# Kernel optimization log

Measured on AMD Instinct MI355X. Metric: run time of the kernel, lower is better.

## Reference

```python
import jax, jax.numpy as jnp
import numpy as np

B, S, D = 2, 2048, 1024
H, DK = 16, 64            # n_heads, d_k = d_model // n_heads
EXP = 4                   # pattern-separation expand_factor
ED = DK * EXP             # expanded_dim = 256
TOPK = 32                 # top-k kept after ReLU expansion
ALPHA = 0.05
TNT = 1.0                 # trace_norm_target


def setup_inputs() -> dict:
    key = jax.random.key(0)
    ks = jax.random.split(key, 8)
    sc = 1.0 / np.sqrt(D)
    x = jax.random.normal(ks[0], (B, S, D), jnp.float32)
    W_q = jax.random.normal(ks[1], (D, D), jnp.float32) * sc
    W_k = jax.random.normal(ks[2], (D, D), jnp.float32) * sc
    W_v = jax.random.normal(ks[3], (D, D), jnp.float32) * sc
    W_o = jax.random.normal(ks[4], (D, D), jnp.float32) * sc
    # trace buffers (non-zero so the trace read path actually matters)
    traces = jax.random.normal(ks[5], (H, DK, DK), jnp.float32) * 0.02
    value_traces = jax.random.normal(ks[6], (H, ED, DK), jnp.float32) * 0.02
    # frozen random expansion projection (dentate gyrus), W / sqrt(d_k)
    W_expand = jax.random.normal(ks[7], (DK, ED), jnp.float32) / np.sqrt(DK)
    return dict(x=x, W_q=W_q, W_k=W_k, W_v=W_v, W_o=W_o,
                traces=traces, value_traces=value_traces, W_expand=W_expand)


def _eff_alpha(T):
    # alpha / (1 + ||T_h||_F / trace_norm_target), shape (1, H, 1, 1)
    norms = jnp.sqrt(jnp.sum(T * T, axis=(1, 2)))
    return (ALPHA / (1.0 + norms / TNT)).reshape(1, -1, 1, 1)


def _forward(x, W_q, W_k, W_v, W_o, traces, value_traces, W_expand):
    b, s, d = x.shape
    def proj(W):
        return jnp.einsum('bsd,de->bse', x, W).reshape(b, s, H, DK).transpose(0, 2, 1, 3)
    Q, K, V = proj(W_q), proj(W_k), proj(W_v)  # (B, H, S, DK)

    scores = jnp.einsum('bhqd,bhkd->bhqk', Q, K)
    # score trace bias: alpha_eff * (Q @ T @ K^T)
    QT = jnp.einsum('bhqd,hde->bhqe', Q, traces)
    trace_scores = jnp.einsum('bhqe,bhke->bhqk', QT, K)
    scores = (scores + _eff_alpha(traces) * trace_scores) / np.sqrt(DK)
    A = jax.nn.softmax(scores, axis=-1)
    out = jnp.einsum('bhqk,bhkd->bhqd', A, V)

    # value trace read with use_key_q shift: address with previous token's Q
    Q_addr = jnp.concatenate([jnp.zeros_like(Q[:, :, :1, :]), Q[:, :, :-1, :]], axis=2)
    # pattern separation: frozen random expansion + ReLU + top-k sparsify
    Q_exp = jax.nn.relu(jnp.einsum('bhsd,de->bhse', Q_addr, W_expand))  # (B,H,S,ED)
    kth = jax.lax.top_k(Q_exp, TOPK)[0][..., -1:]
    Q_sparse = jnp.where(Q_exp >= kth, Q_exp, 0.0)  # == scatter of top-k vals (ties at 0 contribute 0)
    stored = jnp.einsum('bhse,hed->bhsd', Q_sparse, value_traces)
    out = out + _eff_alpha(value_traces) * stored

    out = out.transpose(0, 2, 1, 3).reshape(b, s, d)
    return jnp.einsum('bsd,de->bse', out, W_o)


def reference(x, W_q, W_k, W_v, W_o, traces, value_traces, W_expand):
    return _forward(x, W_q, W_k, W_v, W_o, traces, value_traces, W_expand)
```

## Files before the change

kernel.cpp:

```cpp
#include <hip/hip_runtime.h>
#include <stdint.h>

#define Bn 2
#define Sn 2048
#define Dn 1024
#define Hn 16
#define DKn 64
#define EDn 256

typedef __attribute__((ext_vector_type(8))) short bvec8;
typedef __attribute__((ext_vector_type(4))) float fvec4;

#define MFMA(a, b, c) __builtin_amdgcn_mfma_f32_16x16x32_bf16(a, b, c, 0, 0, 0)

__device__ __forceinline__ float b2f(unsigned short u) {
  return __uint_as_float(((unsigned)u) << 16);
}
__device__ __forceinline__ unsigned short f2b(float x) {
  unsigned u = __float_as_uint(x);
  u += 0x7fffu + ((u >> 16) & 1u);
  return (unsigned short)(u >> 16);
}
__device__ __forceinline__ void g2l(const unsigned short* g, unsigned short* l) {
  __builtin_amdgcn_global_load_lds(
      (const __attribute__((address_space(1))) void*)g,
      (__attribute__((address_space(3))) void*)l, 16, 0, 0);
}

__global__ __launch_bounds__(256) void k_alphas(
    const float* __restrict__ traces, const float* __restrict__ vtr,
    float* __restrict__ alphas) {
  int blk = blockIdx.x;
  const float* base;
  int n;
  if (blk < 16) { base = traces + blk * DKn * DKn; n = DKn * DKn; }
  else          { base = vtr + (blk - 16) * EDn * DKn; n = EDn * DKn; }
  float s = 0.f;
  for (int i = threadIdx.x; i < n; i += 256) { float v = base[i]; s += v * v; }
  __shared__ float red[256];
  red[threadIdx.x] = s;
  __syncthreads();
  for (int off = 128; off > 0; off >>= 1) {
    if (threadIdx.x < off) red[threadIdx.x] += red[threadIdx.x + off];
    __syncthreads();
  }
  if (threadIdx.x == 0) alphas[blk] = 0.05f / (1.f + sqrtf(red[0]));
}

__global__ __launch_bounds__(256) void k_trW(
    const float* __restrict__ w0, const float* __restrict__ w1,
    const float* __restrict__ w2, const float* __restrict__ w3,
    unsigned short* __restrict__ dst) {
  int z = blockIdx.z;
  const float* src = (z == 0) ? w0 : ((z == 1) ? w1 : ((z == 2) ? w2 : w3));
  unsigned short* d = dst + (size_t)z * Dn * Dn;
  __shared__ unsigned short Tl[64][72];
  int tid = threadIdx.x;
  int k0 = blockIdx.y * 64, n0 = blockIdx.x * 64;
#pragma unroll
  for (int i = 0; i < 4; ++i) {
    int q = tid + 256 * i;
    int kr = q >> 4, c4 = q & 15;
    float4 v = *(const float4*)&src[(size_t)(k0 + kr) * Dn + n0 + 4 * c4];
    ushort4 u;
    u.x = f2b(v.x); u.y = f2b(v.y); u.z = f2b(v.z); u.w = f2b(v.w);
    *(ushort4*)&Tl[kr][4 * c4] = u;
  }
  __syncthreads();
#pragma unroll
  for (int i = 0; i < 4; ++i) {
    int q = tid + 256 * i;
    int nr = q >> 4, c4 = q & 15;
    ushort4 u;
    u.x = Tl[4 * c4 + 0][nr]; u.y = Tl[4 * c4 + 1][nr];
    u.z = Tl[4 * c4 + 2][nr]; u.w = Tl[4 * c4 + 3][nr];
    *(ushort4*)&d[(size_t)(n0 + nr) * Dn + k0 + 4 * c4] = u;
  }
}

__global__ __launch_bounds__(256) void k_mkM(const float* __restrict__ tr,
                                             const float* __restrict__ alph,
                                             unsigned short* __restrict__ Mt) {
  int h = blockIdx.x;
  float a = alph[h] * 0.125f;
  const float* th = tr + (size_t)h * DKn * DKn;
  unsigned short* mh = Mt + (size_t)h * DKn * DKn;
  for (int i = threadIdx.x; i < DKn * DKn; i += 256) {
    int e = i >> 6, k = i & 63;
    float v = a * th[(size_t)k * DKn + e] + ((e == k) ? 0.125f : 0.f);
    mh[i] = f2b(v);
  }
}

__global__ __launch_bounds__(256) void k_trE(const float* __restrict__ Wexp,
                                             unsigned short* __restrict__ WexpT) {
  int e0 = blockIdx.x * 64;
  __shared__ unsigned short Tl[64][72];
  int tid = threadIdx.x;
#pragma unroll
  for (int i = 0; i < 4; ++i) {
    int q = tid + 256 * i;
    int dr = q >> 4, c4 = q & 15;
    float4 v = *(const float4*)&Wexp[(size_t)dr * EDn + e0 + 4 * c4];
    ushort4 u;
    u.x = f2b(v.x); u.y = f2b(v.y); u.z = f2b(v.z); u.w = f2b(v.w);
    *(ushort4*)&Tl[dr][4 * c4] = u;
  }
  __syncthreads();
#pragma unroll
  for (int i = 0; i < 4; ++i) {
    int q = tid + 256 * i;
    int er = q >> 4, c4 = q & 15;
    ushort4 u;
    u.x = Tl[4 * c4 + 0][er]; u.y = Tl[4 * c4 + 1][er];
    u.z = Tl[4 * c4 + 2][er]; u.w = Tl[4 * c4 + 3][er];
    *(ushort4*)&WexpT[(size_t)(e0 + er) * DKn + 4 * c4] = u;
  }
}

__global__ __launch_bounds__(256) void k_trVT(const float* __restrict__ vtr,
                                              unsigned short* __restrict__ VTt) {
  int e0 = blockIdx.x * 64;
  int h = blockIdx.y;
  const float* src = vtr + (size_t)h * EDn * DKn;
  unsigned short* dst = VTt + (size_t)h * DKn * EDn;
  __shared__ unsigned short Tl[64][72];
  int tid = threadIdx.x;
#pragma unroll
  for (int i = 0; i < 4; ++i) {
    int q = tid + 256 * i;
    int er = q >> 4, c4 = q & 15;
    float4 v = *(const float4*)&src[(size_t)(e0 + er) * DKn + 4 * c4];
    ushort4 u;
    u.x = f2b(v.x); u.y = f2b(v.y); u.z = f2b(v.z); u.w = f2b(v.w);
    *(ushort4*)&Tl[er][4 * c4] = u;
  }
  __syncthreads();
#pragma unroll
  for (int i = 0; i < 4; ++i) {
    int q = tid + 256 * i;
    int dr = q >> 4, c4 = q & 15;
    ushort4 u;
    u.x = Tl[4 * c4 + 0][dr]; u.y = Tl[4 * c4 + 1][dr];
    u.z = Tl[4 * c4 + 2][dr]; u.w = Tl[4 * c4 + 3][dr];
    *(ushort4*)&dst[(size_t)dr * EDn + e0 + 4 * c4] = u;
  }
}

__global__ __launch_bounds__(256) void k_xb(const float* __restrict__ x,
                                            unsigned short* __restrict__ xb) {
  size_t i = ((size_t)blockIdx.x * 256 + threadIdx.x) * 4;
  float4 v = *(const float4*)&x[i];
  ushort4 u;
  u.x = f2b(v.x); u.y = f2b(v.y); u.z = f2b(v.z); u.w = f2b(v.w);
  *(ushort4*)&xb[i] = u;
}

template <int MODE>
__global__ __launch_bounds__(256) void k_gemm(
    const unsigned short* __restrict__ Ab, const float* __restrict__ Af,
    const unsigned short* __restrict__ BtBase, unsigned short* __restrict__ Qb,
    unsigned short* __restrict__ Kb, unsigned short* __restrict__ VtOut,
    float* __restrict__ Cout) {
  const int z = (MODE == 0) ? blockIdx.z : 0;
  const unsigned short* Bt = BtBase + (size_t)z * Dn * Dn;
  __shared__ unsigned short As[128 * 32];
  __shared__ unsigned short Bs[128 * 32];
  const int tid = threadIdx.x;
  const int w = tid >> 6, lane = tid & 63, qd = lane >> 4, cc = lane & 15;
  const int m0 = blockIdx.y * 128, n0 = blockIdx.x * 128;
  const int mW = 64 * (w >> 1), nW = 64 * (w & 1);
  const int srow = lane >> 2;
  const int schk = 8 * ((lane & 3) ^ (srow & 3));
  const int r0 = 32 * w + srow, r1 = r0 + 16;
  fvec4 acc[4][4];
#pragma unroll
  for (int i = 0; i < 4; ++i)
#pragma unroll
    for (int j = 0; j < 4; ++j) acc[i][j] = (fvec4){0.f, 0.f, 0.f, 0.f};

  for (int k0 = 0; k0 < Dn; k0 += 32) {
    if (MODE == 0) {
      g2l(&Ab[(size_t)(m0 + r0) * Dn + k0 + schk], &As[1024 * w]);
      g2l(&Ab[(size_t)(m0 + r1) * Dn + k0 + schk], &As[1024 * w + 512]);
    } else {
#pragma unroll
      for (int i = 0; i < 4; ++i) {
        int q = tid + 256 * i;
        int row = q >> 3, c4 = q & 7;
        float4 v = *(const float4*)&Af[(size_t)(m0 + row) * Dn + k0 + 4 * c4];
        ushort4 u;
        u.x = f2b(v.x); u.y = f2b(v.y); u.z = f2b(v.z); u.w = f2b(v.w);
        *(ushort4*)&As[row * 32 + 8 * ((c4 >> 1) ^ (row & 3)) + 4 * (c4 & 1)] =
            u;
      }
    }
    g2l(&Bt[(size_t)(n0 + r0) * Dn + k0 + schk], &Bs[1024 * w]);
    g2l(&Bt[(size_t)(n0 + r1) * Dn + k0 + schk], &Bs[1024 * w + 512]);
    __syncthreads();
    bvec8 af[4], bf[4];
#pragma unroll
    for (int i = 0; i < 4; ++i) {
      int ra = mW + 16 * i + cc;
      af[i] = *(const bvec8*)&As[ra * 32 + 8 * (qd ^ (ra & 3))];
      int rb = nW + 16 * i + cc;
      bf[i] = *(const bvec8*)&Bs[rb * 32 + 8 * (qd ^ (rb & 3))];
    }
#pragma unroll
    for (int i = 0; i < 4; ++i)
#pragma unroll
      for (int j = 0; j < 4; ++j) acc[i][j] = MFMA(af[i], bf[j], acc[i][j]);
    __syncthreads();
  }
#pragma unroll
  for (int i = 0; i < 4; ++i)
#pragma unroll
    for (int j = 0; j < 4; ++j) {
      int rowb = m0 + mW + 16 * i + 4 * qd;
      int col = n0 + nW + 16 * j + cc;
      if (MODE == 0) {
        int b = rowb >> 11, s = rowb & 2047;
        int h = col >> 6, dk = col & 63;
        if (z == 2) {
          ushort4 u;
          u.x = f2b(acc[i][j][0]); u.y = f2b(acc[i][j][1]);
          u.z = f2b(acc[i][j][2]); u.w = f2b(acc[i][j][3]);
          *(ushort4*)&VtOut[(((size_t)(b * Hn + h)) * DKn + dk) * Sn + s] = u;
        } else {
          unsigned short* Cb = (z == 0) ? Qb : Kb;
#pragma unroll
          for (int r = 0; r < 4; ++r)
            Cb[(((size_t)(b * Hn + h)) * Sn + s + r) * DKn + dk] =
                f2b(acc[i][j][r]);
        }
      } else {
#pragma unroll
        for (int r = 0; r < 4; ++r)
          Cout[(size_t)(rowb + r) * Dn + col] = acc[i][j][r];
      }
    }
}

__global__ __launch_bounds__(256, 2) void k_pattsep(
    const unsigned short* __restrict__ Qb,
    const unsigned short* __restrict__ WexpT,
    const unsigned short* __restrict__ VTt,
    const float* __restrict__ alphas, float* __restrict__ AT) {
  __shared__ uint4 Wl4[2048];
  __shared__ uint4 Vl4[2048];
  __shared__ uint4 Ps4[4][256];
  const int tile = blockIdx.x, bh = blockIdx.y;
  const int b = bh >> 4, h = bh & 15;
  const int tid = threadIdx.x;
  const int w = tid >> 6, lane = tid & 63, qd = lane >> 4, cc = lane & 15;
  const float avt = alphas[16 + h];

  const uint4* wsrc = (const uint4*)WexpT;
  const uint4* vsrc = (const uint4*)(VTt + (size_t)h * DKn * EDn);
  for (int i = tid; i < 2048; i += 256) {
    int e = i >> 3, c = i & 7;
    Wl4[e * 8 + (c ^ (e & 7))] = wsrc[i];
    int d = i >> 5, c2 = i & 31;
    Vl4[d * 32 + (c2 ^ (d & 7))] = vsrc[i];
  }
  __syncthreads();

  const unsigned short* Wls = (const unsigned short*)Wl4;
  const unsigned short* Vls = (const unsigned short*)Vl4;
  unsigned short* Pw = (unsigned short*)Ps4[w];

  for (int rg = 0; rg < 2; ++rg) {
    const int s0 = tile * 128 + w * 32 + rg * 16;
    bvec8 aq0 = {}, aq1 = {};
    const int srow = s0 + cc;
    if (srow > 0) {
      const unsigned short* qp = Qb + ((size_t)bh * Sn + srow - 1) * DKn;
      aq0 = *(const bvec8*)&qp[8 * qd];
      aq1 = *(const bvec8*)&qp[32 + 8 * qd];
    }
    fvec4 E[16];
#pragma unroll
    for (int j = 0; j < 16; ++j) {
      const int e = 16 * j + cc;
      const unsigned short* wr = Wls + e * 64;
      bvec8 b0 = *(const bvec8*)&wr[8 * (qd ^ (e & 7))];
      bvec8 b1 = *(const bvec8*)&wr[8 * ((4 + qd) ^ (e & 7))];
      fvec4 zv = {0.f, 0.f, 0.f, 0.f};
      zv = MFMA(aq0, b0, zv);
      E[j] = MFMA(aq1, b1, zv);
    }
#pragma unroll
    for (int j = 0; j < 16; ++j)
#pragma unroll
      for (int r = 0; r < 4; ++r) E[j][r] = fmaxf(E[j][r], 0.f);

    float thr[4];
#pragma unroll
    for (int r = 0; r < 4; ++r) {
      unsigned cur = 0u;
      bool done = false;
      for (int bit = 30; bit >= 0; --bit) {
        unsigned cand = cur | (1u << bit);
        float t = __uint_as_float(cand);
        int cnt = 0;
#pragma unroll
        for (int j = 0; j < 16; ++j) cnt += (E[j][r] >= t) ? 1 : 0;
        cnt += __shfl_xor(cnt, 1);
        cnt += __shfl_xor(cnt, 2);
        cnt += __shfl_xor(cnt, 4);
        cnt += __shfl_xor(cnt, 8);
        if (!done && cnt >= 32) {
          cur = cand;
          if (cnt == 32) done = true;
        }
        if (__all(done)) break;
      }
      thr[r] = __uint_as_float(cur);
    }

    fvec4 acc2[4];
#pragma unroll
    for (int j2 = 0; j2 < 4; ++j2) acc2[j2] = (fvec4){0.f, 0.f, 0.f, 0.f};

#pragma unroll
    for (int half = 0; half < 2; ++half) {
#pragma unroll
      for (int j = 0; j < 8; ++j) {
        const int jj = j + 8 * half;
#pragma unroll
        for (int r = 0; r < 4; ++r) {
          float v = E[jj][r];
          bool sel = (v >= thr[r]) && (v > 0.f);
          int row = 4 * qd + r;
          int s = 16 * j + cc;
          int ch = (s >> 3) ^ (row & 7);
          Pw[row * 128 + ch * 8 + (s & 7)] = sel ? f2b(v) : (unsigned short)0;
        }
      }
#pragma unroll
      for (int j2 = 0; j2 < 4; ++j2) {
        const int d = 16 * j2 + cc;
        const unsigned short* vr = Vls + d * 256;
#pragma unroll
        for (int c = 0; c < 4; ++c) {
          int cg = 4 * (c + 4 * half) + qd;
          bvec8 bv = *(const bvec8*)&vr[8 * (cg ^ (d & 7))];
          int ca = 4 * c + qd;
          bvec8 ap = *(const bvec8*)&Pw[cc * 128 + 8 * (ca ^ (cc & 7))];
          acc2[j2] = MFMA(ap, bv, acc2[j2]);
        }
      }
    }
#pragma unroll
    for (int j2 = 0; j2 < 4; ++j2)
#pragma unroll
      for (int r = 0; r < 4; ++r) {
        int row = s0 + 4 * qd + r;
        AT[((size_t)(b * Sn + row)) * Dn + h * DKn + 16 * j2 + cc] =
            avt * acc2[j2][r];
      }
  }
}

__global__ __launch_bounds__(256) void k_attn(
    const unsigned short* __restrict__ Qb, const unsigned short* __restrict__ Kb,
    const unsigned short* __restrict__ Vt, const unsigned short* __restrict__ Mt,
    float* __restrict__ AT) {
  __shared__ unsigned short Kd[64 * 64];
  __shared__ unsigned short Vl[64 * 64];
  __shared__ unsigned short Ps[4][16][72];
  const int bh = blockIdx.x, qt = blockIdx.y;
  const int b = bh >> 4, h = bh & 15;
  const int tid = threadIdx.x;
  const int w = tid >> 6, lane = tid & 63, qd = lane >> 4, cc = lane & 15;
  const float L2E = 1.4426950408889634f;
  const float NB = 23.083120654223414f;

  const unsigned short* qg = Qb + ((size_t)bh * Sn + qt * 64 + w * 16) * DKn;
  bvec8 a0 = *(const bvec8*)&qg[cc * DKn + 8 * qd];
  bvec8 a1 = *(const bvec8*)&qg[cc * DKn + 32 + 8 * qd];
  const unsigned short* mh = Mt + (size_t)h * DKn * DKn;
#pragma unroll
  for (int j = 0; j < 4; ++j) {
    bvec8 b0 = *(const bvec8*)&mh[(size_t)(16 * j + cc) * DKn + 8 * qd];
    bvec8 b1 = *(const bvec8*)&mh[(size_t)(16 * j + cc) * DKn + 32 + 8 * qd];
    fvec4 zz = {0.f, 0.f, 0.f, 0.f};
    zz = MFMA(a0, b0, zz);
    zz = MFMA(a1, b1, zz);
#pragma unroll
    for (int r = 0; r < 4; ++r) {
      int qr = 4 * qd + r;
      Kd[(16 * w + qr) * 64 + 8 * ((2 * j + (cc >> 3)) ^ (qr & 7)) + (cc & 7)] =
          f2b(zz[r]);
    }
  }
  bvec8 aq0 = *(const bvec8*)&Kd[(16 * w + cc) * 64 + 8 * (qd ^ (cc & 7))];
  bvec8 aq1 =
      *(const bvec8*)&Kd[(16 * w + cc) * 64 + 8 * ((qd + 4) ^ (cc & 7))];

  float l_s = 0.f;
  fvec4 O[4];
#pragma unroll
  for (int j = 0; j < 4; ++j) O[j] = (fvec4){0.f, 0.f, 0.f, 0.f};

  const int vrow = lane >> 3;
  const int vchk = 8 * ((lane & 7) ^ (vrow & 7));
  const unsigned short* kgb = Kb + (size_t)bh * Sn * DKn;
  const unsigned short* vgb = Vt + (size_t)bh * DKn * Sn;

  for (int kt = 0; kt < Sn / 64; ++kt) {
    __syncthreads();
    const unsigned short* kg = kgb + (size_t)kt * 64 * DKn;
    g2l(&kg[(size_t)(16 * w + vrow) * 64 + vchk], &Kd[1024 * w]);
    g2l(&kg[(size_t)(16 * w + 8 + vrow) * 64 + vchk], &Kd[1024 * w + 512]);
    g2l(&vgb[(size_t)(16 * w + vrow) * Sn + kt * 64 + vchk], &Vl[1024 * w]);
    g2l(&vgb[(size_t)(16 * w + 8 + vrow) * Sn + kt * 64 + vchk],
        &Vl[1024 * w + 512]);
    __syncthreads();
    fvec4 sc[4];
#pragma unroll
    for (int j = 0; j < 4; ++j) {
      int rk = 16 * j + cc;
      bvec8 b0 = *(const bvec8*)&Kd[rk * 64 + 8 * (qd ^ (cc & 7))];
      bvec8 b1 = *(const bvec8*)&Kd[rk * 64 + 8 * ((qd + 4) ^ (cc & 7))];
      fvec4 zz = {0.f, 0.f, 0.f, 0.f};
      zz = MFMA(b0, aq0, zz);
      sc[j] = MFMA(b1, aq1, zz);
    }
#pragma unroll
    for (int j = 0; j < 4; ++j) {
      float p0 = __builtin_amdgcn_exp2f(fmaf(sc[j][0], L2E, -NB));
      float p1 = __builtin_amdgcn_exp2f(fmaf(sc[j][1], L2E, -NB));
      float p2 = __builtin_amdgcn_exp2f(fmaf(sc[j][2], L2E, -NB));
      float p3 = __builtin_amdgcn_exp2f(fmaf(sc[j][3], L2E, -NB));
      l_s += (p0 + p1) + (p2 + p3);
      ushort4 u;
      u.x = f2b(p0); u.y = f2b(p1); u.z = f2b(p2); u.w = f2b(p3);
      *(ushort4*)&Ps[w][cc][16 * j + 4 * qd] = u;
    }
    bvec8 ap0 = *(const bvec8*)&Ps[w][cc][8 * qd];
    bvec8 ap1 = *(const bvec8*)&Ps[w][cc][32 + 8 * qd];
#pragma unroll
    for (int j = 0; j < 4; ++j) {
      int rv = 16 * j + cc;
      bvec8 v0 = *(const bvec8*)&Vl[rv * 64 + 8 * (qd ^ (cc & 7))];
      bvec8 v1 = *(const bvec8*)&Vl[rv * 64 + 8 * ((qd + 4) ^ (cc & 7))];
      O[j] = MFMA(ap0, v0, O[j]);
      O[j] = MFMA(ap1, v1, O[j]);
    }
  }
  l_s += __shfl_xor(l_s, 16);
  l_s += __shfl_xor(l_s, 32);
  float linv = 1.f / l_s;
  float inv[4];
#pragma unroll
  for (int r = 0; r < 4; ++r) inv[r] = __shfl(linv, 4 * qd + r);
#pragma unroll
  for (int j = 0; j < 4; ++j)
#pragma unroll
    for (int r = 0; r < 4; ++r) {
      int row = qt * 64 + w * 16 + 4 * qd + r;
      float* p = AT + ((size_t)(b * Sn + row)) * Dn + h * DKn + 16 * j + cc;
      *p += O[j][r] * inv[r];
    }
}

extern "C" void kernel_launch(void* const* d_in, const int* in_sizes, int n_in,
                              void* d_out, int out_size, void* d_ws,
                              size_t ws_size, hipStream_t stream) {
  const float* x = (const float*)d_in[0];
  const float* Wq = (const float*)d_in[1];
  const float* Wk = (const float*)d_in[2];
  const float* Wv = (const float*)d_in[3];
  const float* Wo = (const float*)d_in[4];
  const float* traces = (const float*)d_in[5];
  const float* vtr = (const float*)d_in[6];
  const float* Wexp = (const float*)d_in[7];

  const size_t NQ = (size_t)Bn * Hn * Sn * DKn;
  unsigned short* Qb = (unsigned short*)d_ws;
  unsigned short* Kb = Qb + NQ;
  unsigned short* Vt = Kb + NQ;
  unsigned short* Wt = Vt + NQ;
  unsigned short* Mt = Wt + NQ;
  unsigned short* WexpT = Mt + 65536;
  unsigned short* VTt = WexpT + 16384;
  float* alph = (float*)(VTt + 262144);
  float* AT = alph + 32;
  unsigned short* xb = (unsigned short*)AT;

  k_alphas<<<32, 256, 0, stream>>>(traces, vtr, alph);
  k_trW<<<dim3(16, 16, 4), 256, 0, stream>>>(Wq, Wk, Wv, Wo, Wt);
  k_mkM<<<16, 256, 0, stream>>>(traces, alph, Mt);
  k_trE<<<4, 256, 0, stream>>>(Wexp, WexpT);
  k_trVT<<<dim3(4, 16), 256, 0, stream>>>(vtr, VTt);
  k_xb<<<4096, 256, 0, stream>>>(x, xb);
  k_gemm<0><<<dim3(8, 32, 3), 256, 0, stream>>>(xb, nullptr, Wt, Qb, Kb, Vt,
                                                nullptr);
  k_pattsep<<<dim3(16, 32), 256, 0, stream>>>(Qb, WexpT, VTt, alph, AT);
  k_attn<<<dim3(32, 32), 256, 0, stream>>>(Qb, Kb, Vt, Mt, AT);
  k_gemm<1><<<dim3(8, 32, 1), 256, 0, stream>>>(
      nullptr, AT, Wt + 3 * (size_t)Dn * Dn, nullptr, nullptr, nullptr,
      (float*)d_out);
}
```

Measured before the change: 313.1 us.

## Double-buffer K/V tiles in attention kernel and pack P conversion

The attention kernel now double-buffers the K and V tiles in LDS. It prefetches the next tile with global_load_lds while computing on the current one, and needs only one barrier per iteration instead of two. The P tile store also changes: it uses the hardware packed bf16 conversion instruction and an XOR-swizzled layout with no padding, which cuts conversion ALU work and LDS bank conflicts. This doubles LDS use for K/V, which may lower occupancy.

```diff
diff --git a/kernel.cpp b/kernel.cpp
--- a/kernel.cpp
+++ b/kernel.cpp
@@ -366,9 +366,9 @@
     const unsigned short* __restrict__ Qb, const unsigned short* __restrict__ Kb,
     const unsigned short* __restrict__ Vt, const unsigned short* __restrict__ Mt,
     float* __restrict__ AT) {
-  __shared__ unsigned short Kd[64 * 64];
-  __shared__ unsigned short Vl[64 * 64];
-  __shared__ unsigned short Ps[4][16][72];
+  __shared__ unsigned short Kd[2][64 * 64];
+  __shared__ unsigned short Vl[2][64 * 64];
+  __shared__ unsigned short Ps[4][16 * 64];
   const int bh = blockIdx.x, qt = blockIdx.y;
   const int b = bh >> 4, h = bh & 15;
   const int tid = threadIdx.x;
@@ -380,6 +380,7 @@
   bvec8 a0 = *(const bvec8*)&qg[cc * DKn + 8 * qd];
   bvec8 a1 = *(const bvec8*)&qg[cc * DKn + 32 + 8 * qd];
   const unsigned short* mh = Mt + (size_t)h * DKn * DKn;
+  unsigned short* Ksc = Kd[0];
 #pragma unroll
   for (int j = 0; j < 4; ++j) {
     bvec8 b0 = *(const bvec8*)&mh[(size_t)(16 * j + cc) * DKn + 8 * qd];
@@ -390,13 +391,14 @@
 #pragma unroll
     for (int r = 0; r < 4; ++r) {
       int qr = 4 * qd + r;
-      Kd[(16 * w + qr) * 64 + 8 * ((2 * j + (cc >> 3)) ^ (qr & 7)) + (cc & 7)] =
+      Ksc[(16 * w + qr) * 64 + 8 * ((2 * j + (cc >> 3)) ^ (qr & 7)) + (cc & 7)] =
           f2b(zz[r]);
     }
   }
-  bvec8 aq0 = *(const bvec8*)&Kd[(16 * w + cc) * 64 + 8 * (qd ^ (cc & 7))];
+  bvec8 aq0 = *(const bvec8*)&Ksc[(16 * w + cc) * 64 + 8 * (qd ^ (cc & 7))];
   bvec8 aq1 =
-      *(const bvec8*)&Kd[(16 * w + cc) * 64 + 8 * ((qd + 4) ^ (cc & 7))];
+      *(const bvec8*)&Ksc[(16 * w + cc) * 64 + 8 * ((qd + 4) ^ (cc & 7))];
+  asm volatile("s_waitcnt lgkmcnt(0)" ::: "memory");
 
   float l_s = 0.f;
   fvec4 O[4];
@@ -408,25 +410,41 @@
   const unsigned short* kgb = Kb + (size_t)bh * Sn * DKn;
   const unsigned short* vgb = Vt + (size_t)bh * DKn * Sn;
 
-  for (int kt = 0; kt < Sn / 64; ++kt) {
-    __syncthreads();
-    const unsigned short* kg = kgb + (size_t)kt * 64 * DKn;
-    g2l(&kg[(size_t)(16 * w + vrow) * 64 + vchk], &Kd[1024 * w]);
-    g2l(&kg[(size_t)(16 * w + 8 + vrow) * 64 + vchk], &Kd[1024 * w + 512]);
-    g2l(&vgb[(size_t)(16 * w + vrow) * Sn + kt * 64 + vchk], &Vl[1024 * w]);
-    g2l(&vgb[(size_t)(16 * w + 8 + vrow) * Sn + kt * 64 + vchk],
-        &Vl[1024 * w + 512]);
-    __syncthreads();
+  g2l(&kgb[(size_t)(16 * w + vrow) * 64 + vchk], &Kd[0][1024 * w]);
+  g2l(&kgb[(size_t)(16 * w + 8 + vrow) * 64 + vchk], &Kd[0][1024 * w + 512]);
+  g2l(&vgb[(size_t)(16 * w + vrow) * Sn + vchk], &Vl[0][1024 * w]);
+  g2l(&vgb[(size_t)(16 * w + 8 + vrow) * Sn + vchk], &Vl[0][1024 * w + 512]);
+
+  const int NT = Sn / 64;
+  for (int kt = 0; kt < NT; ++kt) {
+    const int buf = kt & 1;
+    asm volatile("s_waitcnt vmcnt(0)" ::: "memory");
+    __builtin_amdgcn_s_barrier();
+    if (kt + 1 < NT) {
+      const unsigned short* kg = kgb + (size_t)(kt + 1) * 64 * DKn;
+      unsigned short* Kn = Kd[buf ^ 1];
+      unsigned short* Vn = Vl[buf ^ 1];
+      g2l(&kg[(size_t)(16 * w + vrow) * 64 + vchk], &Kn[1024 * w]);
+      g2l(&kg[(size_t)(16 * w + 8 + vrow) * 64 + vchk], &Kn[1024 * w + 512]);
+      g2l(&vgb[(size_t)(16 * w + vrow) * Sn + (kt + 1) * 64 + vchk],
+          &Vn[1024 * w]);
+      g2l(&vgb[(size_t)(16 * w + 8 + vrow) * Sn + (kt + 1) * 64 + vchk],
+          &Vn[1024 * w + 512]);
+    }
+    __builtin_amdgcn_sched_barrier(0);
+    const unsigned short* Kc = Kd[buf];
+    const unsigned short* Vc = Vl[buf];
     fvec4 sc[4];
 #pragma unroll
     for (int j = 0; j < 4; ++j) {
       int rk = 16 * j + cc;
-      bvec8 b0 = *(const bvec8*)&Kd[rk * 64 + 8 * (qd ^ (cc & 7))];
-      bvec8 b1 = *(const bvec8*)&Kd[rk * 64 + 8 * ((qd + 4) ^ (cc & 7))];
+      bvec8 b0 = *(const bvec8*)&Kc[rk * 64 + 8 * (qd ^ (cc & 7))];
+      bvec8 b1 = *(const bvec8*)&Kc[rk * 64 + 8 * ((qd + 4) ^ (cc & 7))];
       fvec4 zz = {0.f, 0.f, 0.f, 0.f};
       zz = MFMA(b0, aq0, zz);
       sc[j] = MFMA(b1, aq1, zz);
     }
+    unsigned short* Pw = Ps[w];
 #pragma unroll
     for (int j = 0; j < 4; ++j) {
       float p0 = __builtin_amdgcn_exp2f(fmaf(sc[j][0], L2E, -NB));
@@ -434,17 +452,24 @@
       float p2 = __builtin_amdgcn_exp2f(fmaf(sc[j][2], L2E, -NB));
       float p3 = __builtin_amdgcn_exp2f(fmaf(sc[j][3], L2E, -NB));
       l_s += (p0 + p1) + (p2 + p3);
-      ushort4 u;
-      u.x = f2b(p0); u.y = f2b(p1); u.z = f2b(p2); u.w = f2b(p3);
-      *(ushort4*)&Ps[w][cc][16 * j + 4 * qd] = u;
-    }
-    bvec8 ap0 = *(const bvec8*)&Ps[w][cc][8 * qd];
-    bvec8 ap1 = *(const bvec8*)&Ps[w][cc][32 + 8 * qd];
+      unsigned q01, q23;
+      asm("v_cvt_pk_bf16_f32 %0, %1, %2" : "=v"(q01) : "v"(p0), "v"(p1));
+      asm("v_cvt_pk_bf16_f32 %0, %1, %2" : "=v"(q23) : "v"(p2), "v"(p3));
+      uint2 uu;
+      uu.x = q01; uu.y = q23;
+      *(uint2*)&Pw[cc * 64 + 4 * ((4 * j + qd) ^ cc)] = uu;
+    }
+    union U16 { bvec8 v; uint2 u[2]; } U0, U1;
+    U0.u[0] = *(const uint2*)&Pw[cc * 64 + 4 * ((2 * qd) ^ cc)];
+    U0.u[1] = *(const uint2*)&Pw[cc * 64 + 4 * ((2 * qd + 1) ^ cc)];
+    U1.u[0] = *(const uint2*)&Pw[cc * 64 + 4 * ((8 + 2 * qd) ^ cc)];
+    U1.u[1] = *(const uint2*)&Pw[cc * 64 + 4 * ((9 + 2 * qd) ^ cc)];
+    bvec8 ap0 = U0.v, ap1 = U1.v;
 #pragma unroll
     for (int j = 0; j < 4; ++j) {
       int rv = 16 * j + cc;
-      bvec8 v0 = *(const bvec8*)&Vl[rv * 64 + 8 * (qd ^ (cc & 7))];
-      bvec8 v1 = *(const bvec8*)&Vl[rv * 64 + 8 * ((qd + 4) ^ (cc & 7))];
+      bvec8 v0 = *(const bvec8*)&Vc[rv * 64 + 8 * (qd ^ (cc & 7))];
+      bvec8 v1 = *(const bvec8*)&Vc[rv * 64 + 8 * ((qd + 4) ^ (cc & 7))];
       O[j] = MFMA(ap0, v0, O[j]);
       O[j] = MFMA(ap1, v1, O[j]);
     }
```

Result: no change. 308.3 us (-1.6%).
